# Optimization experiments

Hardware: AMD Instinct MI355X
Metric: run time of the kernel (lower is better)

The kernel has to match this reference:

```python
import jax, jax.numpy as jnp
import numpy as np

C = 1024      # channels
H = 16        # num_heads
D = C // H    # head_dim = 64
K = 64        # max_kernel_size
MAX_FREQ = 16.0
MIN_FREQ = 1.0
HALF_S = 16   # from max_samples=32, ndim=1 -> offsets -16..16 (S=33)
MAX_RECEPTIVE = HALF_S * MAX_FREQ  # 256.0
EPS = 1e-6


def rmsnorm(x, w):
    # LlamaRMSNorm: fp32 accumulation, scale by learned gamma
    xf = x.astype(jnp.float32)
    var = jnp.mean(xf * xf, axis=-1, keepdims=True)
    return (w * (xf * jax.lax.rsqrt(var + EPS))).astype(x.dtype)


def setup_inputs() -> dict:
    key = jax.random.key(0)
    ks = jax.random.split(key, 7)
    B, L = 2, 2048
    return {
        "x": jax.random.normal(ks[0], (B, L, C), jnp.float32),
        "w_wave": jax.random.normal(ks[1], (2 * H, C), jnp.float32) * 0.02,
        "b_wave": jax.random.normal(ks[2], (2 * H,), jnp.float32) * 0.02,
        "g_wave": jnp.ones((2 * H,), jnp.float32),
        "w_kern": jax.random.normal(ks[3], (H * K, C), jnp.float32) * 0.02,
        "b_kern": jnp.zeros((H * K,), jnp.float32),
        "g_kern": jnp.ones((H * K,), jnp.float32),
        "w_exp": jax.random.normal(ks[4], (1, C), jnp.float32) * 0.02,
        "b_exp": jnp.zeros((1,), jnp.float32),
        "g_exp": jnp.ones((1,), jnp.float32),
        "w_out": jax.random.normal(ks[5], (C, C), jnp.float32) * 0.02,
    }


def reference(x, w_wave, b_wave, g_wave, w_kern, b_kern, g_kern,
              w_exp, b_exp, g_exp, w_out):
    B, L, _ = x.shape
    dt = x.dtype
    offsets = jnp.arange(-HALF_S, HALF_S + 1, dtype=dt)  # (S,) S=33

    # wave params -> per-token, per-head freq & phase
    wave = jax.nn.silu(rmsnorm(x @ w_wave.T + b_wave, g_wave)).reshape(B, L, 2, H)
    freq = jax.nn.sigmoid(wave[:, :, 0]) * (MAX_FREQ - MIN_FREQ) + MIN_FREQ  # (B,L,H)
    phase = jnp.tanh(wave[:, :, 1]) * MAX_FREQ                               # (B,L,H)

    # learned sample positions with bilinear (linear in 1D) interpolation
    centers = jnp.arange(L, dtype=dt)
    pos = centers[None, :, None, None] + offsets * freq[..., None] + phase[..., None]  # (B,L,H,S)
    valid = ((pos >= 0) & (pos < L)).astype(dt)
    pc = jnp.clip(pos, 0.0, L - 1.001)
    fl = jnp.clip(jnp.floor(pc).astype(jnp.int32), 0, L - 1)
    cl = jnp.minimum(fl + 1, L - 1)
    frac = pc - fl.astype(dt)
    rel = offsets * freq[..., None]  # (B,L,H,S)

    # per-token kernel projection + interpolation to sample positions
    kernel_max = jax.nn.silu(rmsnorm(x @ w_kern.T + b_kern, g_kern)).reshape(B, L, H, K)
    exponent = jax.nn.sigmoid(rmsnorm(x @ w_exp.T + b_exp, g_exp)) * 3.5 + 0.5  # (B,L,1)
    power = 1.0 / jnp.power(1.0 + jnp.abs(rel) / L, exponent[..., None])        # (B,L,H,S)

    idx_f = jnp.clip(jnp.abs(rel) / MAX_RECEPTIVE, 0.0, 1.0) * (K - 1)
    i0 = jnp.clip(idx_f.astype(jnp.int32), 0, K - 2)
    i1 = i0 + 1
    wc = idx_f - i0.astype(dt)
    wf = 1.0 - wc
    k0 = jnp.take_along_axis(kernel_max, i0, axis=-1)
    k1 = jnp.take_along_axis(kernel_max, i1, axis=-1)
    kern = (k0 * wf + k1 * wc) * power * valid  # (B,L,H,S)

    # gather values at floor/ceil positions and interpolate
    xh = x.reshape(B, L, H, D)
    bidx = jnp.arange(B)[:, None, None, None]
    hidx = jnp.arange(H)[None, None, :, None]
    vf = xh[bidx, fl, hidx]  # (B,L,H,S,D)
    vc = xh[bidx, cl, hidx]
    val = vf * (1.0 - frac[..., None]) + vc * frac[..., None]

    hidden = jnp.einsum('blhs,blhsd->blhd', kern, val).reshape(B, L, C)
    return jax.nn.silu(hidden @ w_out.T)
```

## Files before the change

kernel.cpp:

```cpp
#include <hip/hip_runtime.h>
#include <hip/hip_bf16.h>
#include <math.h>

#define B_ 2
#define L_ 2048
#define C_ 1024
#define H_ 16
#define D_ 64
#define K_ 64
#define S_ 33
#define M_ (B_*L_)

typedef _Float16 half8 __attribute__((ext_vector_type(8)));
typedef float f32x4 __attribute__((ext_vector_type(4)));

__device__ __forceinline__ float sigmoidf_(float v) { return 1.f / (1.f + __expf(-v)); }

__global__ __launch_bounds__(256) void conv_w(
    const float* __restrict__ w_kern, const float* __restrict__ w_out,
    _Float16* __restrict__ wkh, _Float16* __restrict__ woh)
{
  int i = blockIdx.x * 256 + threadIdx.x;
  const float* src; _Float16* dst; int j;
  if (i < 131072) { src = w_kern; dst = wkh; j = i; }
  else            { src = w_out;  dst = woh; j = i - 131072; }
  float4 a = ((const float4*)src)[j * 2];
  float4 b = ((const float4*)src)[j * 2 + 1];
  half8 v;
  v[0] = (_Float16)a.x; v[1] = (_Float16)a.y; v[2] = (_Float16)a.z; v[3] = (_Float16)a.w;
  v[4] = (_Float16)b.x; v[5] = (_Float16)b.y; v[6] = (_Float16)b.z; v[7] = (_Float16)b.w;
  ((half8*)dst)[j] = v;
}

__global__ __launch_bounds__(256) void prep(
    const float* __restrict__ x,
    const float* __restrict__ w_wave, const float* __restrict__ b_wave,
    const float* __restrict__ g_wave,
    const float* __restrict__ w_exp, const float* __restrict__ b_exp,
    const float* __restrict__ g_exp,
    _Float16* __restrict__ xh,
    float* __restrict__ freq, float* __restrict__ phase, float* __restrict__ expn)
{
  __shared__ float xs[4 * C_];
  __shared__ float dots[4][S_];
  int bid = blockIdx.x;
  int tid = threadIdx.x;
  int lane = tid & 63, wv = tid >> 6;
  int m0 = bid * 4;

#pragma unroll
  for (int q = 0; q < 4; q++) {
    int idx = tid + q * 256;
    ((float4*)xs)[idx] = ((const float4*)(x + (size_t)m0 * C_))[idx];
  }
  __syncthreads();

#pragma unroll
  for (int q = 0; q < 2; q++) {
    int i8 = tid + q * 256;
    float4 a = ((const float4*)xs)[i8 * 2];
    float4 b = ((const float4*)xs)[i8 * 2 + 1];
    half8 v;
    v[0] = (_Float16)a.x; v[1] = (_Float16)a.y; v[2] = (_Float16)a.z; v[3] = (_Float16)a.w;
    v[4] = (_Float16)b.x; v[5] = (_Float16)b.y; v[6] = (_Float16)b.z; v[7] = (_Float16)b.w;
    ((half8*)(xh + (size_t)m0 * C_))[i8] = v;
  }

  const float* xrow = xs + wv * C_;
  for (int n = 0; n < 33; n++) {
    const float* wr = (n < 32) ? (w_wave + n * C_) : w_exp;
    float s = 0.f;
#pragma unroll
    for (int q = 0; q < 4; q++) {
      int k4 = lane + q * 64;
      float4 xv = ((const float4*)xrow)[k4];
      float4 wv4 = ((const float4*)wr)[k4];
      s += xv.x * wv4.x + xv.y * wv4.y + xv.z * wv4.z + xv.w * wv4.w;
    }
    for (int o = 32; o; o >>= 1) s += __shfl_xor(s, o);
    if (lane == 0) dots[wv][n] = s + ((n < 32) ? b_wave[n] : b_exp[0]);
  }
  __syncthreads();

  int m = m0 + wv;
  float v = (lane < 32) ? dots[wv][lane] : 0.f;
  float ss = v * v;
  for (int o = 32; o; o >>= 1) ss += __shfl_xor(ss, o);
  float scale = rsqrtf(ss * (1.f / 32.f) + 1e-6f);
  if (lane < 32) {
    float nv = dots[wv][lane] * scale * g_wave[lane];
    float sv = nv * sigmoidf_(nv);
    if (lane < 16) freq[m * H_ + lane] = sigmoidf_(sv) * 15.f + 1.f;
    else           phase[m * H_ + lane - 16] = tanhf(sv) * 16.f;
  }
  if (lane == 0) {
    float y = dots[wv][32];
    float nv = y * rsqrtf(y * y + 1e-6f) * g_exp[0];
    expn[m] = sigmoidf_(nv) * 3.5f + 0.5f;
  }
}

__global__ __launch_bounds__(256) void gemm_sk(
    const _Float16* __restrict__ A, const _Float16* __restrict__ Bw,
    _Float16* __restrict__ Cp, int M, int N, int Kd)
{
  __shared__ __align__(16) _Float16 As[128 * 32];
  __shared__ __align__(16) _Float16 Bs[128 * 32];
  int tid = threadIdx.x;
  int m0 = blockIdx.y * 128, n0 = blockIdx.x * 128;
  int z = blockIdx.z;
  int kbase = z * (Kd >> 1);
  int lane = tid & 63;
  int wid = tid >> 6, wm = wid >> 1, wn = wid & 1;

  f32x4 acc[4][4];
#pragma unroll
  for (int i = 0; i < 4; i++)
#pragma unroll
    for (int j = 0; j < 4; j++)
      acc[i][j] = (f32x4){0.f, 0.f, 0.f, 0.f};

  for (int k0 = 0; k0 < (Kd >> 1); k0 += 32) {
#pragma unroll
    for (int q = 0; q < 2; q++) {
      int idx = tid + q * 256;
      int row = idx >> 2, seg = idx & 3;
      int sseg = seg ^ (row & 3);
      const _Float16* ga = A  + (size_t)(m0 + row) * Kd + kbase + k0 + sseg * 8;
      const _Float16* gb = Bw + (size_t)(n0 + row) * Kd + kbase + k0 + sseg * 8;
      __builtin_amdgcn_global_load_lds(
          (const __attribute__((address_space(1))) unsigned int*)ga,
          (__attribute__((address_space(3))) unsigned int*)&As[idx * 8], 16, 0, 0);
      __builtin_amdgcn_global_load_lds(
          (const __attribute__((address_space(1))) unsigned int*)gb,
          (__attribute__((address_space(3))) unsigned int*)&Bs[idx * 8], 16, 0, 0);
    }
    __syncthreads();

    half8 aF[4], bF[4];
#pragma unroll
    for (int i = 0; i < 4; i++) {
      int ar = wm * 64 + i * 16 + (lane & 15);
      int ac = (lane >> 4) ^ (ar & 3);
      aF[i] = *(const half8*)&As[ar * 32 + ac * 8];
    }
#pragma unroll
    for (int j = 0; j < 4; j++) {
      int br = wn * 64 + j * 16 + (lane & 15);
      int bc = (lane >> 4) ^ (br & 3);
      bF[j] = *(const half8*)&Bs[br * 32 + bc * 8];
    }
#pragma unroll
    for (int i = 0; i < 4; i++)
#pragma unroll
      for (int j = 0; j < 4; j++)
        acc[i][j] = __builtin_amdgcn_mfma_f32_16x16x32_f16(aF[i], bF[j], acc[i][j], 0, 0, 0);
    __syncthreads();
  }

  _Float16* Cz = Cp + (size_t)z * M * N;
#pragma unroll
  for (int i = 0; i < 4; i++)
#pragma unroll
    for (int j = 0; j < 4; j++) {
      int col = n0 + wn * 64 + j * 16 + (lane & 15);
#pragma unroll
      for (int r = 0; r < 4; r++) {
        int row = m0 + wm * 64 + i * 16 + (lane >> 4) * 4 + r;
        Cz[(size_t)row * N + col] = (_Float16)acc[i][j][r];
      }
    }
}

__global__ __launch_bounds__(256) void epi(
    const _Float16* __restrict__ hp, float* __restrict__ out)
{
  int i = blockIdx.x * 256 + threadIdx.x;
  half8 a = ((const half8*)hp)[i];
  half8 b = ((const half8*)(hp + (size_t)M_ * C_))[i];
  float o[8];
#pragma unroll
  for (int j = 0; j < 8; j++) {
    float t = (float)a[j] + (float)b[j];
    o[j] = t * sigmoidf_(t);
  }
  ((float4*)out)[i * 2]     = make_float4(o[0], o[1], o[2], o[3]);
  ((float4*)out)[i * 2 + 1] = make_float4(o[4], o[5], o[6], o[7]);
}

__global__ __launch_bounds__(256) void sampler(
    const _Float16* __restrict__ xh, const _Float16* __restrict__ ykp,
    const float* __restrict__ b_kern, const float* __restrict__ g_kern,
    const float* __restrict__ freq, const float* __restrict__ phase,
    const float* __restrict__ expn, _Float16* __restrict__ hidden)
{
  __shared__ float km[2][C_];
  __shared__ float kw[2][H_][S_];
  __shared__ float fr[2][H_][S_];
  __shared__ int   fli[2][H_][S_];
  __shared__ float red2[2][2];
  int bid = blockIdx.x;
  int pair = ((bid & 7) << 8) + (bid >> 3);
  int tid = threadIdx.x;
  int sub = tid >> 7, t = tid & 127;
  int m = pair * 2 + sub;
  int b = m >> 11, l = m & (L_ - 1);
  int lane = tid & 63;

  float yv[8];
  {
    half8 h0 = *(const half8*)(ykp + (size_t)m * C_ + t * 8);
    half8 h1 = *(const half8*)(ykp + (size_t)M_ * C_ + (size_t)m * C_ + t * 8);
    float ss = 0.f;
#pragma unroll
    for (int j = 0; j < 8; j++) {
      yv[j] = (float)h0[j] + (float)h1[j] + b_kern[t * 8 + j];
      ss += yv[j] * yv[j];
    }
    for (int o = 32; o; o >>= 1) ss += __shfl_xor(ss, o);
    if (lane == 0) red2[sub][t >> 6] = ss;
  }
  __syncthreads();
  {
    float scale = rsqrtf((red2[sub][0] + red2[sub][1]) * (1.f / 1024.f) + 1e-6f);
#pragma unroll
    for (int j = 0; j < 8; j++) {
      float nv = yv[j] * scale * g_kern[t * 8 + j];
      km[sub][t * 8 + j] = nv * sigmoidf_(nv);
    }
  }
  __syncthreads();

  float e = expn[m];
  for (int i = t; i < H_ * S_; i += 128) {
    int h = i / S_, s = i - h * S_;
    float f  = freq[m * H_ + h];
    float ph = phase[m * H_ + h];
    float rel = (float)(s - 16) * f;
    float posv = (float)l + rel + ph;
    float kern = 0.f, frac = 0.f;
    int fl = 0;
    if (posv >= 0.f && posv < 2048.f) {
      float pc = fminf(posv, 2046.999f);
      fl = (int)pc;
      frac = pc - (float)fl;
      float ar = fabsf(rel);
      float idx_f = fminf(ar * (1.f / 256.f), 1.f) * 63.f;
      int i0 = (int)idx_f; if (i0 > 62) i0 = 62;
      float wc = idx_f - (float)i0;
      float k0 = km[sub][(h << 6) + i0];
      float k1 = km[sub][(h << 6) + i0 + 1];
      float powv = __expf(-e * __logf(1.f + ar * (1.f / 2048.f)));
      kern = (k0 * (1.f - wc) + k1 * wc) * powv;
    }
    kw[sub][h][s] = kern; fr[sub][h][s] = frac; fli[sub][h][s] = fl;
  }
  __syncthreads();

  int h = t >> 3, d8 = (t & 7) << 3;
  const _Float16* xb = xh + (size_t)b * L_ * C_ + (h << 6) + d8;
  float acc[8] = {0.f, 0.f, 0.f, 0.f, 0.f, 0.f, 0.f, 0.f};
#pragma unroll 4
  for (int s = 0; s < S_; s++) {
    float kern = kw[sub][h][s];
    float frac = fr[sub][h][s];
    int fl = fli[sub][h][s];
    const _Float16* pf = xb + (size_t)fl * C_;
    half8 vf = *(const half8*)pf;
    half8 vc = *(const half8*)(pf + C_);
    float wf = kern * (1.f - frac), wcf = kern * frac;
#pragma unroll
    for (int j = 0; j < 8; j++)
      acc[j] += wf * (float)vf[j] + wcf * (float)vc[j];
  }
  half8 o8;
#pragma unroll
  for (int j = 0; j < 8; j++) o8[j] = (_Float16)acc[j];
  *(half8*)(hidden + (size_t)m * C_ + (h << 6) + d8) = o8;
}

extern "C" void kernel_launch(void* const* d_in, const int* in_sizes, int n_in,
                              void* d_out, int out_size, void* d_ws, size_t ws_size,
                              hipStream_t stream) {
  const float* x      = (const float*)d_in[0];
  const float* w_wave = (const float*)d_in[1];
  const float* b_wave = (const float*)d_in[2];
  const float* g_wave = (const float*)d_in[3];
  const float* w_kern = (const float*)d_in[4];
  const float* b_kern = (const float*)d_in[5];
  const float* g_kern = (const float*)d_in[6];
  const float* w_exp  = (const float*)d_in[7];
  const float* b_exp  = (const float*)d_in[8];
  const float* g_exp  = (const float*)d_in[9];
  const float* w_out  = (const float*)d_in[10];
  float* out = (float*)d_out;

  char* ws = (char*)d_ws;
  _Float16* xhp    = (_Float16*)ws;
  _Float16* hidden = (_Float16*)(ws + (size_t) 8 * 1024 * 1024);
  _Float16* ykp    = (_Float16*)(ws + (size_t)16 * 1024 * 1024);
  _Float16* hp     = (_Float16*)(ws + (size_t)32 * 1024 * 1024);
  _Float16* wkh    = (_Float16*)(ws + (size_t)48 * 1024 * 1024);
  _Float16* woh    = (_Float16*)(ws + (size_t)50 * 1024 * 1024);
  float*    freqb  = (float*)(ws + (size_t)52 * 1024 * 1024);
  float*    phaseb = freqb + (size_t)M_ * H_;
  float*    expnb  = phaseb + (size_t)M_ * H_;

  conv_w<<<1024, 256, 0, stream>>>(w_kern, w_out, wkh, woh);
  prep<<<M_ / 4, 256, 0, stream>>>(x, w_wave, b_wave, g_wave, w_exp, b_exp, g_exp,
                                   xhp, freqb, phaseb, expnb);
  dim3 gg(C_ / 128, M_ / 128, 2);
  gemm_sk<<<gg, 256, 0, stream>>>(xhp, wkh, ykp, M_, C_, C_);
  sampler<<<M_ / 2, 256, 0, stream>>>(xhp, ykp, b_kern, g_kern,
                                      freqb, phaseb, expnb, hidden);
  gemm_sk<<<gg, 256, 0, stream>>>(hidden, woh, hp, M_, C_, C_);
  epi<<<(M_ * C_) / 2048, 256, 0, stream>>>(hp, out);
}
```

Measured before the change: 187.0 us.

## Double-buffer GEMM LDS tiles and use packed fp16 accumulation in gather kernel

The split-K GEMM now keeps two LDS buffers and issues the global-to-LDS loads for the next K tile before computing on the current one, so load latency can overlap the MFMA work. The gather/interpolation kernel moves its inner multiply-accumulate to packed half8 fp16 arithmetic, flushing into fp32 accumulators every four samples, and fully unrolls the sample loop. The fp16 partial sums reduce precision. Because the next tile's async LDS loads are not waited on before the barrier, the GEMM could read incomplete data.

```diff
diff --git a/kernel.cpp b/kernel.cpp
--- a/kernel.cpp
+++ b/kernel.cpp
@@ -104,8 +104,8 @@
     const _Float16* __restrict__ A, const _Float16* __restrict__ Bw,
     _Float16* __restrict__ Cp, int M, int N, int Kd)
 {
-  __shared__ __align__(16) _Float16 As[128 * 32];
-  __shared__ __align__(16) _Float16 Bs[128 * 32];
+  __shared__ __align__(16) _Float16 As[2][128 * 32];
+  __shared__ __align__(16) _Float16 Bs[2][128 * 32];
   int tid = threadIdx.x;
   int m0 = blockIdx.y * 128, n0 = blockIdx.x * 128;
   int z = blockIdx.z;
@@ -120,7 +120,7 @@
     for (int j = 0; j < 4; j++)
       acc[i][j] = (f32x4){0.f, 0.f, 0.f, 0.f};
 
-  for (int k0 = 0; k0 < (Kd >> 1); k0 += 32) {
+  auto STAGE = [&](int buf, int k0) {
 #pragma unroll
     for (int q = 0; q < 2; q++) {
       int idx = tid + q * 256;
@@ -130,32 +130,41 @@
       const _Float16* gb = Bw + (size_t)(n0 + row) * Kd + kbase + k0 + sseg * 8;
       __builtin_amdgcn_global_load_lds(
           (const __attribute__((address_space(1))) unsigned int*)ga,
-          (__attribute__((address_space(3))) unsigned int*)&As[idx * 8], 16, 0, 0);
+          (__attribute__((address_space(3))) unsigned int*)&As[buf][idx * 8], 16, 0, 0);
       __builtin_amdgcn_global_load_lds(
           (const __attribute__((address_space(1))) unsigned int*)gb,
-          (__attribute__((address_space(3))) unsigned int*)&Bs[idx * 8], 16, 0, 0);
-    }
-    __syncthreads();
+          (__attribute__((address_space(3))) unsigned int*)&Bs[buf][idx * 8], 16, 0, 0);
+    }
+  };
+
+  const int nt = (Kd >> 1) / 32;
+  STAGE(0, 0);
+  __syncthreads();
+  int cur = 0;
+  for (int t = 0; t < nt; t++) {
+    if (t + 1 < nt) STAGE(cur ^ 1, (t + 1) * 32);
 
     half8 aF[4], bF[4];
 #pragma unroll
     for (int i = 0; i < 4; i++) {
       int ar = wm * 64 + i * 16 + (lane & 15);
       int ac = (lane >> 4) ^ (ar & 3);
-      aF[i] = *(const half8*)&As[ar * 32 + ac * 8];
+      aF[i] = *(const half8*)&As[cur][ar * 32 + ac * 8];
     }
 #pragma unroll
     for (int j = 0; j < 4; j++) {
       int br = wn * 64 + j * 16 + (lane & 15);
       int bc = (lane >> 4) ^ (br & 3);
-      bF[j] = *(const half8*)&Bs[br * 32 + bc * 8];
+      bF[j] = *(const half8*)&Bs[cur][br * 32 + bc * 8];
     }
 #pragma unroll
     for (int i = 0; i < 4; i++)
 #pragma unroll
       for (int j = 0; j < 4; j++)
         acc[i][j] = __builtin_amdgcn_mfma_f32_16x16x32_f16(aF[i], bF[j], acc[i][j], 0, 0, 0);
+
     __syncthreads();
+    cur ^= 1;
   }
 
   _Float16* Cz = Cp + (size_t)z * M * N;
@@ -259,8 +268,12 @@
 
   int h = t >> 3, d8 = (t & 7) << 3;
   const _Float16* xb = xh + (size_t)b * L_ * C_ + (h << 6) + d8;
-  float acc[8] = {0.f, 0.f, 0.f, 0.f, 0.f, 0.f, 0.f, 0.f};
-#pragma unroll 4
+  float accf[8] = {0.f, 0.f, 0.f, 0.f, 0.f, 0.f, 0.f, 0.f};
+  half8 hzero;
+#pragma unroll
+  for (int j = 0; j < 8; j++) hzero[j] = (_Float16)0.f;
+  half8 acch = hzero;
+#pragma unroll
   for (int s = 0; s < S_; s++) {
     float kern = kw[sub][h][s];
     float frac = fr[sub][h][s];
@@ -268,14 +281,21 @@
     const _Float16* pf = xb + (size_t)fl * C_;
     half8 vf = *(const half8*)pf;
     half8 vc = *(const half8*)(pf + C_);
-    float wf = kern * (1.f - frac), wcf = kern * frac;
-#pragma unroll
-    for (int j = 0; j < 8; j++)
-      acc[j] += wf * (float)vf[j] + wcf * (float)vc[j];
-  }
+    _Float16 wfh = (_Float16)(kern * (1.f - frac));
+    _Float16 wch = (_Float16)(kern * frac);
+    acch = acch + vf * wfh + vc * wch;
+    if ((s & 3) == 3) {
+#pragma unroll
+      for (int j = 0; j < 8; j++) accf[j] += (float)acch[j];
+      acch = hzero;
+    }
+  }
+#pragma unroll
+  for (int j = 0; j < 8; j++) accf[j] += (float)acch[j];
+
   half8 o8;
 #pragma unroll
-  for (int j = 0; j < 8; j++) o8[j] = (_Float16)acc[j];
+  for (int j = 0; j < 8; j++) o8[j] = (_Float16)accf[j];
   *(half8*)(hidden + (size_t)m * C_ + (h << 6) + d8) = o8;
 }
 
```

Measured after the change: 181.8 us. 1.03x faster.
